# Optimization experiments

Hardware: AMD Instinct MI355X
Metric: run time of the kernel (lower is better)

Reference implementation:

```python
import jax, jax.numpy as jnp
import numpy as np

N_MODES = 64


def setup_inputs() -> dict:
    key = jax.random.key(0)
    ks = jax.random.split(key, 5)
    B, L, C, M = 32, 8192, 64, N_MODES
    scale = 1.0 / (C * M)
    return {
        "x": jax.random.normal(ks[0], (B, L, C), dtype=jnp.float32),
        "w_spec_real": jax.random.normal(ks[1], (C, C, M), dtype=jnp.float32) * scale,
        "w_spec_imag": jax.random.normal(ks[2], (C, C, M), dtype=jnp.float32) * scale,
        "pw_weight": jax.random.normal(ks[3], (C, C), dtype=jnp.float32) * (1.0 / np.sqrt(C)),
        "pw_bias": jax.random.normal(ks[4], (C,), dtype=jnp.float32) * 0.01,
    }


def reference(x, w_spec_real, w_spec_imag, pw_weight, pw_bias):
    # x: [B, L, C] -> [B, C, L] (matches torch transpose(1, 2))
    xt = jnp.swapaxes(x, 1, 2)
    L = xt.shape[-1]
    xf = jnp.fft.rfft(xt, axis=-1)            # [B, C, F] complex64, F = L//2 + 1
    F = xf.shape[-1]
    K = min(N_MODES, F)
    W = (w_spec_real + 1j * w_spec_imag).astype(xf.dtype)  # [Cin, Cout, M]
    # Batched replacement of the per-mode loop: [B,Cin,K] x [Cin,Cout,K] -> [B,Cout,K]
    tf_low = jnp.einsum('bik,iok->bok', xf[:, :, :K], W[:, :, :K])
    tf = jnp.zeros_like(xf).at[:, :, :K].set(tf_low)
    x_back = jnp.fft.irfft(tf, n=L, axis=-1)  # [B, C, L] real
    # pointwise conv (kernel_size=1): [Cout,Cin] x [B,Cin,L] + bias
    pw = jnp.einsum('oi,bil->bol', pw_weight, xt) + pw_bias[None, :, None]
    return jnp.swapaxes(x_back + pw, 1, 2)     # [B, L, C]
```

## Files before the change

kernel.cpp:

```cpp
#include <hip/hip_runtime.h>
#include <stdint.h>

#define L_     8192
#define NB     32
#define NC     64
#define SPLITK 16
#define CHUNK  (L_ / SPLITK)
#define SXPAD  520

#define BF_OFF  0
#define XF_OFF  (2u  << 20)
#define XR_OFF  (18u << 20)
#define TF_OFF  (19u << 20)

typedef __bf16 bf16x8 __attribute__((ext_vector_type(8)));
typedef float  f32x4  __attribute__((ext_vector_type(4)));

__device__ __forceinline__ unsigned short f2bf(float f) {
  union { float f; unsigned int i; } v; v.f = f;
  unsigned int r = v.i + 0x7fffu + ((v.i >> 16) & 1u);
  return (unsigned short)(r >> 16);
}
__device__ __forceinline__ f32x4 mfma16(bf16x8 a, bf16x8 b, f32x4 c) {
  return __builtin_amdgcn_mfma_f32_16x16x32_bf16(a, b, c, 0, 0, 0);
}

__global__ __launch_bounds__(256) void k0_bf(unsigned short* __restrict__ Bf) {
  const int e0 = (blockIdx.x * 256 + threadIdx.x) * 8;
  const int j = e0 >> 13, l0 = e0 & 8191, k = j >> 1;
  const float W0 = 6.283185307179586f / 8192.0f;
  const float a = (k == 0 ? 1.0f : 2.0f) * (1.0f / 8192.0f);
  uint32_t w[4];
  #pragma unroll
  for (int u = 0; u < 4; ++u) {
    float s0, c0, s1, c1;
    __sincosf((float)((k * (l0 + 2 * u)) & 8191) * W0, &s0, &c0);
    __sincosf((float)((k * (l0 + 2 * u + 1)) & 8191) * W0, &s1, &c1);
    const unsigned short b0 = f2bf((j & 1) ? (-a * s0) : (a * c0));
    const unsigned short b1 = f2bf((j & 1) ? (-a * s1) : (a * c1));
    w[u] = (uint32_t)b0 | ((uint32_t)b1 << 16);
  }
  uint4 v; v.x = w[0]; v.y = w[1]; v.z = w[2]; v.w = w[3];
  *(uint4*)(Bf + e0) = v;
}

__global__ __launch_bounds__(256) void k1_dft(const float* __restrict__ x,
                                              const unsigned short* __restrict__ Bf,
                                              float* __restrict__ XFP) {
  const int b = blockIdx.x >> 5;
  const int p = (blockIdx.x >> 1) & 15;
  const int h = blockIdx.x & 1;
  const int l0 = p * CHUNK;
  const int t = threadIdx.x;
  const int wv = t >> 6, lane = t & 63, q = lane >> 4, n = lane & 15;
  __shared__ uint32_t sx[32 * (SXPAD / 2)];
  const float* xb = x + (size_t)b * L_ * NC + h * 32;

  {
    const int g  = t & 7;
    const int r2 = t >> 3;
    #pragma unroll
    for (int s = 0; s < 8; ++s) {
      const int lp = s * 32 + r2;
      const f32x4 u0 = *(const f32x4*)(xb + (size_t)(l0 + 2 * lp) * NC + 4 * g);
      const f32x4 u1 = *(const f32x4*)(xb + (size_t)(l0 + 2 * lp + 1) * NC + 4 * g);
      #pragma unroll
      for (int jj = 0; jj < 4; ++jj) {
        __bf16 pk2[2] = {(__bf16)u0[jj], (__bf16)u1[jj]};
        sx[(4 * g + jj) * (SXPAD / 2) + lp] = __builtin_bit_cast(uint32_t, pk2);
      }
    }
  }
  __syncthreads();

  f32x4 acc[2][2];
  #pragma unroll
  for (int i = 0; i < 2; ++i)
    #pragma unroll
    for (int jn = 0; jn < 2; ++jn) acc[i][jn] = (f32x4){0.f, 0.f, 0.f, 0.f};
  const unsigned short* sxu = (const unsigned short*)sx;

  for (int ks = 0; ks < CHUNK; ks += 32) {
    const int lb = ks + q * 8;
    const bf16x8 bfr0 = *(const bf16x8*)(sxu + (n)      * SXPAD + lb);
    const bf16x8 bfr1 = *(const bf16x8*)(sxu + (16 + n) * SXPAD + lb);
    #pragma unroll
    for (int mt = 0; mt < 2; ++mt) {
      const bf16x8 afr = *(const bf16x8*)(Bf + (size_t)(wv * 32 + mt * 16 + n) * L_ + l0 + lb);
      acc[mt][0] = mfma16(afr, bfr0, acc[mt][0]);
      acc[mt][1] = mfma16(afr, bfr1, acc[mt][1]);
    }
  }

  float* op = XFP + (size_t)(p * NB + b) * 8192;
  #pragma unroll
  for (int mt = 0; mt < 2; ++mt)
    #pragma unroll
    for (int nt = 0; nt < 2; ++nt)
      *(f32x4*)(op + (size_t)(h * 32 + nt * 16 + n) * 128 + (wv * 32 + mt * 16 + q * 4)) =
          acc[mt][nt];
}

__global__ __launch_bounds__(256) void k1b_red(const f32x4* __restrict__ XFP,
                                               f32x4* __restrict__ XFR) {
  const int idx = blockIdx.x * 256 + threadIdx.x;
  f32x4 s = XFP[idx];
  #pragma unroll
  for (int p = 1; p < SPLITK; ++p) {
    const f32x4 v = XFP[(size_t)p * 65536 + idx];
    s[0] += v[0]; s[1] += v[1]; s[2] += v[2]; s[3] += v[3];
  }
  XFR[idx] = s;
}

__global__ __launch_bounds__(256) void k2_mix(const float* __restrict__ XFR,
                                              const float* __restrict__ wr,
                                              const float* __restrict__ wi,
                                              const float* __restrict__ pww,
                                              uint32_t* __restrict__ tf_stage) {
  const int b = blockIdx.x >> 4;
  const int og = blockIdx.x & 15;
  const int t = threadIdx.x;
  const int k = t & 63;
  const int wv = t >> 6;
  const int o = og * 4 + wv;
  const float2* xfb = (const float2*)(XFR + (size_t)b * 8192);
  float ar = 0.f, ai = 0.f;
  #pragma unroll 8
  for (int i = 0; i < 64; ++i) {
    const float2 xv  = xfb[i * 64 + k];
    const float  wrv = wr[(size_t)i * 4096 + o * 64 + k];
    const float  wiv = wi[(size_t)i * 4096 + o * 64 + k];
    ar = fmaf(xv.x, wrv, ar);  ar = fmaf(-xv.y, wiv, ar);
    ai = fmaf(xv.x, wiv, ai);  ai = fmaf(xv.y, wrv, ai);
  }
  uint32_t* row = tf_stage + ((size_t)b * 64 + o) * 96;
  row[k] = (uint32_t)f2bf(ar) | ((uint32_t)f2bf(ai) << 16);
  if (k < 32)
    row[64 + k] = (uint32_t)f2bf(pww[o * 64 + 2 * k]) |
                  ((uint32_t)f2bf(pww[o * 64 + 2 * k + 1]) << 16);
}

__global__ __launch_bounds__(256) void k2b_copy(const uint4* __restrict__ src,
                                                uint4* __restrict__ dst) {
  const int idx = blockIdx.x * 256 + threadIdx.x;
  dst[idx] = src[idx];
}

__global__ __launch_bounds__(256) void k3_out(const float* __restrict__ x,
                                              const unsigned short* __restrict__ tf,
                                              const float* __restrict__ bias,
                                              float* __restrict__ out) {
  const int b = blockIdx.x >> 6;
  const int lt = blockIdx.x & 63;
  const int wv = threadIdx.x >> 6;
  const int lane = threadIdx.x & 63;
  const int q = lane >> 4;
  const int n = lane & 15;
  const int l0 = lt * 128 + wv * 32;
  const float* xb = x + (size_t)b * L_ * NC;
  const unsigned short* tfb = tf + (size_t)b * 64 * 192;
  const float W0 = 6.283185307179586f / 8192.0f;
  f32x4 acc[4][2];
  #pragma unroll
  for (int i = 0; i < 4; ++i)
    #pragma unroll
    for (int jn = 0; jn < 2; ++jn) acc[i][jn] = (f32x4){0.f, 0.f, 0.f, 0.f};
  const int lA = l0 + n;
  const int lB = l0 + 16 + n;
  #pragma unroll
  for (int s = 0; s < 6; ++s) {
    const int k0 = s * 32;
    bf16x8 b0, b1;
    if (s < 4) {
      #pragma unroll
      for (int jj = 0; jj < 4; ++jj) {
        const int kf = (k0 >> 1) + q * 4 + jj;
        float sv, cv;
        __sincosf((float)((kf * lA) & 8191) * W0, &sv, &cv);
        b0[2 * jj] = (__bf16)cv; b0[2 * jj + 1] = (__bf16)(-sv);
        __sincosf((float)((kf * lB) & 8191) * W0, &sv, &cv);
        b1[2 * jj] = (__bf16)cv; b1[2 * jj + 1] = (__bf16)(-sv);
      }
    } else {
      const int cc = (k0 - 128) + q * 8;
      const f32x4* p0 = (const f32x4*)(xb + (size_t)lA * NC + cc);
      const f32x4* p1 = (const f32x4*)(xb + (size_t)lB * NC + cc);
      const f32x4 u00 = p0[0], u01 = p0[1], u10 = p1[0], u11 = p1[1];
      #pragma unroll
      for (int jj = 0; jj < 4; ++jj) {
        b0[jj] = (__bf16)u00[jj]; b0[4 + jj] = (__bf16)u01[jj];
        b1[jj] = (__bf16)u10[jj]; b1[4 + jj] = (__bf16)u11[jj];
      }
    }
    #pragma unroll
    for (int mt = 0; mt < 4; ++mt) {
      const bf16x8 afr = *(const bf16x8*)(tfb + (size_t)(mt * 16 + n) * 192 + k0 + q * 8);
      acc[mt][0] = mfma16(afr, b0, acc[mt][0]);
      acc[mt][1] = mfma16(afr, b1, acc[mt][1]);
    }
  }
  float* ob = out + (size_t)b * L_ * NC;
  #pragma unroll
  for (int mt = 0; mt < 4; ++mt) {
    const f32x4 bv = *(const f32x4*)(bias + mt * 16 + q * 4);
    #pragma unroll
    for (int nt = 0; nt < 2; ++nt) {
      const int l = l0 + nt * 16 + n;
      f32x4 v = acc[mt][nt];
      v[0] += bv[0]; v[1] += bv[1]; v[2] += bv[2]; v[3] += bv[3];
      *(f32x4*)(ob + (size_t)l * NC + mt * 16 + q * 4) = v;
    }
  }
}

extern "C" void kernel_launch(void* const* d_in, const int* in_sizes, int n_in,
                              void* d_out, int out_size, void* d_ws, size_t ws_size,
                              hipStream_t stream) {
  (void)in_sizes; (void)n_in; (void)out_size; (void)d_ws; (void)ws_size;
  const float* x    = (const float*)d_in[0];
  float*       wr   = (float*)d_in[1];
  const float* wi   = (const float*)d_in[2];
  const float* pww  = (const float*)d_in[3];
  const float* bias = (const float*)d_in[4];
  float* out = (float*)d_out;

  char* ob = (char*)d_out;
  unsigned short* Bf  = (unsigned short*)(ob + BF_OFF);
  float*          XFP = (float*)(ob + XF_OFF);
  float*          XFR = (float*)(ob + XR_OFF);
  uint32_t*       TFS = (uint32_t*)(ob + TF_OFF);

  k0_bf   <<<512,             256, 0, stream>>>(Bf);
  k1_dft  <<<NB * SPLITK * 2, 256, 0, stream>>>(x, Bf, XFP);
  k1b_red <<<256,             256, 0, stream>>>((const f32x4*)XFP, (f32x4*)XFR);
  k2_mix  <<<NB * 16,         256, 0, stream>>>(XFR, wr, wi, pww, TFS);
  k2b_copy<<<192,             256, 0, stream>>>((const uint4*)TFS, (uint4*)wr);
  k3_out  <<<NB * 64,         256, 0, stream>>>(x, (const unsigned short*)wr, bias, out);
}
```

Before: 200.9 us.

## Widen DFT blocks to all channels and stage spectral tile in LDS

The forward DFT kernel now has each block cover all 64 channels instead of half, so each bf16 twiddle row read from global memory feeds twice as many MFMAs. The block count halves and LDS per block doubles. The output kernel loads its x rows at kernel start, before the sincos work, to hide latency, and stages the per-batch mixed-spectrum tile in padded shared memory instead of reading it from global for each MFMA. These changes raise register and LDS pressure and lower occupancy.

```diff
diff --git a/kernel.cpp b/kernel.cpp
--- a/kernel.cpp
+++ b/kernel.cpp
@@ -47,48 +47,49 @@
 __global__ __launch_bounds__(256) void k1_dft(const float* __restrict__ x,
                                               const unsigned short* __restrict__ Bf,
                                               float* __restrict__ XFP) {
-  const int b = blockIdx.x >> 5;
-  const int p = (blockIdx.x >> 1) & 15;
-  const int h = blockIdx.x & 1;
+  const int b = blockIdx.x >> 4;
+  const int p = blockIdx.x & 15;
   const int l0 = p * CHUNK;
   const int t = threadIdx.x;
   const int wv = t >> 6, lane = t & 63, q = lane >> 4, n = lane & 15;
-  __shared__ uint32_t sx[32 * (SXPAD / 2)];
-  const float* xb = x + (size_t)b * L_ * NC + h * 32;
+  __shared__ uint32_t sx[NC * SXPAD / 2];
+  const float* xb = x + (size_t)b * L_ * NC;
 
   {
-    const int g  = t & 7;
-    const int r2 = t >> 3;
-    #pragma unroll
-    for (int s = 0; s < 8; ++s) {
-      const int lp = s * 32 + r2;
-      const f32x4 u0 = *(const f32x4*)(xb + (size_t)(l0 + 2 * lp) * NC + 4 * g);
-      const f32x4 u1 = *(const f32x4*)(xb + (size_t)(l0 + 2 * lp + 1) * NC + 4 * g);
+    const int g  = t & 15;
+    const int r2 = t >> 4;
+    for (int s = 0; s < 16; ++s) {
+      const int lrow = s * 32 + 2 * r2;
+      const f32x4 u0 = *(const f32x4*)(xb + (size_t)(l0 + lrow) * NC + 4 * g);
+      const f32x4 u1 = *(const f32x4*)(xb + (size_t)(l0 + lrow + 1) * NC + 4 * g);
       #pragma unroll
       for (int jj = 0; jj < 4; ++jj) {
         __bf16 pk2[2] = {(__bf16)u0[jj], (__bf16)u1[jj]};
-        sx[(4 * g + jj) * (SXPAD / 2) + lp] = __builtin_bit_cast(uint32_t, pk2);
+        sx[(4 * g + jj) * (SXPAD / 2) + s * 16 + r2] = __builtin_bit_cast(uint32_t, pk2);
       }
     }
   }
   __syncthreads();
 
-  f32x4 acc[2][2];
+  f32x4 acc[2][4];
   #pragma unroll
   for (int i = 0; i < 2; ++i)
     #pragma unroll
-    for (int jn = 0; jn < 2; ++jn) acc[i][jn] = (f32x4){0.f, 0.f, 0.f, 0.f};
+    for (int jn = 0; jn < 4; ++jn) acc[i][jn] = (f32x4){0.f, 0.f, 0.f, 0.f};
   const unsigned short* sxu = (const unsigned short*)sx;
 
   for (int ks = 0; ks < CHUNK; ks += 32) {
     const int lb = ks + q * 8;
-    const bf16x8 bfr0 = *(const bf16x8*)(sxu + (n)      * SXPAD + lb);
-    const bf16x8 bfr1 = *(const bf16x8*)(sxu + (16 + n) * SXPAD + lb);
+    bf16x8 bfr[4];
+    #pragma unroll
+    for (int nt = 0; nt < 4; ++nt)
+      bfr[nt] = *(const bf16x8*)(sxu + (nt * 16 + n) * SXPAD + lb);
     #pragma unroll
     for (int mt = 0; mt < 2; ++mt) {
       const bf16x8 afr = *(const bf16x8*)(Bf + (size_t)(wv * 32 + mt * 16 + n) * L_ + l0 + lb);
-      acc[mt][0] = mfma16(afr, bfr0, acc[mt][0]);
-      acc[mt][1] = mfma16(afr, bfr1, acc[mt][1]);
+      #pragma unroll
+      for (int nt = 0; nt < 4; ++nt)
+        acc[mt][nt] = mfma16(afr, bfr[nt], acc[mt][nt]);
     }
   }
 
@@ -96,8 +97,8 @@
   #pragma unroll
   for (int mt = 0; mt < 2; ++mt)
     #pragma unroll
-    for (int nt = 0; nt < 2; ++nt)
-      *(f32x4*)(op + (size_t)(h * 32 + nt * 16 + n) * 128 + (wv * 32 + mt * 16 + q * 4)) =
+    for (int nt = 0; nt < 4; ++nt)
+      *(f32x4*)(op + (size_t)(nt * 16 + n) * 128 + (wv * 32 + mt * 16 + q * 4)) =
           acc[mt][nt];
 }
 
@@ -153,21 +154,46 @@
                                               float* __restrict__ out) {
   const int b = blockIdx.x >> 6;
   const int lt = blockIdx.x & 63;
-  const int wv = threadIdx.x >> 6;
-  const int lane = threadIdx.x & 63;
+  const int t = threadIdx.x;
+  const int wv = t >> 6;
+  const int lane = t & 63;
   const int q = lane >> 4;
   const int n = lane & 15;
   const int l0 = lt * 128 + wv * 32;
   const float* xb = x + (size_t)b * L_ * NC;
   const unsigned short* tfb = tf + (size_t)b * 64 * 192;
   const float W0 = 6.283185307179586f / 8192.0f;
-  f32x4 acc[4][2];
-  #pragma unroll
-  for (int i = 0; i < 4; ++i)
-    #pragma unroll
-    for (int jn = 0; jn < 2; ++jn) acc[i][jn] = (f32x4){0.f, 0.f, 0.f, 0.f};
   const int lA = l0 + n;
   const int lB = l0 + 16 + n;
+
+  const f32x4* pA0 = (const f32x4*)(xb + (size_t)lA * NC + q * 8);
+  const f32x4* pB0 = (const f32x4*)(xb + (size_t)lB * NC + q * 8);
+  const f32x4* pA1 = (const f32x4*)(xb + (size_t)lA * NC + 32 + q * 8);
+  const f32x4* pB1 = (const f32x4*)(xb + (size_t)lB * NC + 32 + q * 8);
+  const f32x4 xA00 = pA0[0], xA01 = pA0[1];
+  const f32x4 xB00 = pB0[0], xB01 = pB0[1];
+  const f32x4 xA10 = pA1[0], xA11 = pA1[1];
+  const f32x4 xB10 = pB1[0], xB11 = pB1[1];
+
+  __shared__ unsigned short stf[64 * 200];
+  {
+    uint4* dst = (uint4*)stf;
+    const uint4* src = (const uint4*)tfb;
+    #pragma unroll
+    for (int i = 0; i < 6; ++i) {
+      const int e4 = t + i * 256;
+      const int row = e4 / 24, c4 = e4 - row * 24;
+      dst[row * 25 + c4] = src[e4];
+    }
+  }
+  __syncthreads();
+
+  f32x4 acc[4][2];
+  #pragma unroll
+  for (int i = 0; i < 4; ++i)
+    #pragma unroll
+    for (int jn = 0; jn < 2; ++jn) acc[i][jn] = (f32x4){0.f, 0.f, 0.f, 0.f};
+
   #pragma unroll
   for (int s = 0; s < 6; ++s) {
     const int k0 = s * 32;
@@ -182,20 +208,22 @@
         __sincosf((float)((kf * lB) & 8191) * W0, &sv, &cv);
         b1[2 * jj] = (__bf16)cv; b1[2 * jj + 1] = (__bf16)(-sv);
       }
+    } else if (s == 4) {
+      #pragma unroll
+      for (int jj = 0; jj < 4; ++jj) {
+        b0[jj] = (__bf16)xA00[jj]; b0[4 + jj] = (__bf16)xA01[jj];
+        b1[jj] = (__bf16)xB00[jj]; b1[4 + jj] = (__bf16)xB01[jj];
+      }
     } else {
-      const int cc = (k0 - 128) + q * 8;
-      const f32x4* p0 = (const f32x4*)(xb + (size_t)lA * NC + cc);
-      const f32x4* p1 = (const f32x4*)(xb + (size_t)lB * NC + cc);
-      const f32x4 u00 = p0[0], u01 = p0[1], u10 = p1[0], u11 = p1[1];
-      #pragma unroll
-      for (int jj = 0; jj < 4; ++jj) {
-        b0[jj] = (__bf16)u00[jj]; b0[4 + jj] = (__bf16)u01[jj];
-        b1[jj] = (__bf16)u10[jj]; b1[4 + jj] = (__bf16)u11[jj];
+      #pragma unroll
+      for (int jj = 0; jj < 4; ++jj) {
+        b0[jj] = (__bf16)xA10[jj]; b0[4 + jj] = (__bf16)xA11[jj];
+        b1[jj] = (__bf16)xB10[jj]; b1[4 + jj] = (__bf16)xB11[jj];
       }
     }
     #pragma unroll
     for (int mt = 0; mt < 4; ++mt) {
-      const bf16x8 afr = *(const bf16x8*)(tfb + (size_t)(mt * 16 + n) * 192 + k0 + q * 8);
+      const bf16x8 afr = *(const bf16x8*)(stf + (mt * 16 + n) * 200 + k0 + q * 8);
       acc[mt][0] = mfma16(afr, b0, acc[mt][0]);
       acc[mt][1] = mfma16(afr, b1, acc[mt][1]);
     }
@@ -231,10 +259,10 @@
   float*          XFR = (float*)(ob + XR_OFF);
   uint32_t*       TFS = (uint32_t*)(ob + TF_OFF);
 
-  k0_bf   <<<512,             256, 0, stream>>>(Bf);
-  k1_dft  <<<NB * SPLITK * 2, 256, 0, stream>>>(x, Bf, XFP);
-  k1b_red <<<256,             256, 0, stream>>>((const f32x4*)XFP, (f32x4*)XFR);
-  k2_mix  <<<NB * 16,         256, 0, stream>>>(XFR, wr, wi, pww, TFS);
-  k2b_copy<<<192,             256, 0, stream>>>((const uint4*)TFS, (uint4*)wr);
-  k3_out  <<<NB * 64,         256, 0, stream>>>(x, (const unsigned short*)wr, bias, out);
-}
+  k0_bf   <<<512,         256, 0, stream>>>(Bf);
+  k1_dft  <<<NB * SPLITK, 256, 0, stream>>>(x, Bf, XFP);
+  k1b_red <<<256,         256, 0, stream>>>((const f32x4*)XFP, (f32x4*)XFR);
+  k2_mix  <<<NB * 16,     256, 0, stream>>>(XFR, wr, wi, pww, TFS);
+  k2b_copy<<<192,         256, 0, stream>>>((const uint4*)TFS, (uint4*)wr);
+  k3_out  <<<NB * 64,     256, 0, stream>>>(x, (const unsigned short*)wr, bias, out);
+}
```

Measured after the change: 184.9 us. -7.9%, faster.
